# Kernel optimization log

Hardware: AMD Instinct MI355X
Metric: run time of the kernel (lower is better)

Reference implementation:

```python
import jax, jax.numpy as jnp
import numpy as np
from jax import lax

B, L, E_DIM, KSZ = 4, 256, 200, 3
VOCAB, N_LABELS, CORNET = 50000, 28415, 1000
N_EDGES = 454640


def setup_inputs() -> dict:
    key = jax.random.key(0)
    ks = jax.random.split(key, 32)
    w = lambda k, shape, s=0.02: jax.random.normal(k, shape, jnp.float32) * s
    inp = {}
    for i, name in enumerate(['abstract', 'intro', 'method', 'results', 'discuss']):
        inp[name] = jax.random.randint(ks[i], (B, L), 0, VOCAB, dtype=jnp.int32)
    inp['src'] = jax.random.randint(ks[5], (N_EDGES,), 0, N_LABELS, dtype=jnp.int32)
    inp['dst'] = jax.random.randint(ks[6], (N_EDGES,), 0, N_LABELS, dtype=jnp.int32)
    inp['g_node_feature'] = w(ks[7], (N_LABELS, E_DIM))
    inp['emb'] = w(ks[8], (VOCAB, E_DIM))
    for j in range(3):
        inp[f'conv_w{j+1}'] = w(ks[9 + j], (E_DIM, E_DIM, KSZ), 0.05)
        inp[f'conv_b{j+1}'] = jnp.zeros((E_DIM,), jnp.float32)
    inp['gcn_w1'] = w(ks[12], (E_DIM, E_DIM))
    inp['gcn_b1'] = jnp.zeros((E_DIM,), jnp.float32)
    inp['gcn_w2'] = w(ks[13], (E_DIM, E_DIM))
    inp['gcn_b2'] = jnp.zeros((E_DIM,), jnp.float32)
    for blk in (1, 2):
        inp[f'cor_wd{blk}'] = w(ks[13 + blk * 2], (CORNET, N_LABELS), 0.01)
        inp[f'cor_bd{blk}'] = jnp.zeros((CORNET,), jnp.float32)
        inp[f'cor_wc{blk}'] = w(ks[14 + blk * 2], (N_LABELS, CORNET), 0.01)
        inp[f'cor_bc{blk}'] = jnp.zeros((N_LABELS,), jnp.float32)
    return inp


def _conv1d(x, wgt, b, dil):
    # x: [B, C, L]; wgt: [O, I, K]; VALID padding, dilation=dil; SELU (dropout in eval mode)
    y = lax.conv_general_dilated(x, wgt, window_strides=(1,), padding='VALID',
                                 rhs_dilation=(dil,), dimension_numbers=('NCH', 'OIH', 'NCH'))
    return jax.nn.selu(y + b[None, :, None])


def _gcn_agg(feat, src, dst, n):
    # DGL copy_src + sum: h[d] = sum over edges (s->d) of feat[s]
    return jax.ops.segment_sum(feat[src], dst, num_segments=n)


def reference(abstract, intro, method, results, discuss, src, dst, g_node_feature,
              emb, conv_w1, conv_b1, conv_w2, conv_b2, conv_w3, conv_b3,
              gcn_w1, gcn_b1, gcn_w2, gcn_b2,
              cor_wd1, cor_bd1, cor_wc1, cor_bc1, cor_wd2, cor_bd2, cor_wc2, cor_bc2):
    n = g_node_feature.shape[0]
    # LabelNet: two GCN layers (sum-aggregate then linear), relu in between
    h = _gcn_agg(g_node_feature, src, dst, n) @ gcn_w1.T + gcn_b1
    h = jax.nn.relu(h)
    h = _gcn_agg(h, src, dst, n) @ gcn_w2.T + gcn_b2
    label_feature = h + g_node_feature  # [N, E]

    def stream(tokens):
        x = emb[tokens]                      # [B, L, E]
        x = jnp.transpose(x, (0, 2, 1))      # [B, E, L]
        x = _conv1d(x, conv_w1, conv_b1, 1)
        x = _conv1d(x, conv_w2, conv_b2, 2)
        x = _conv1d(x, conv_w3, conv_b3, 3)  # [B, E, L']
        scores = jnp.einsum('bel,ne->bln', x, label_feature)  # [B, L', N]
        atten = jax.nn.softmax(scores, axis=1)                # softmax over L' (dim=1 in torch)
        return jnp.einsum('bel,bln->bne', x, atten)           # [B, N, E]

    context = stream(abstract) + stream(intro) + stream(method) + stream(results) + stream(discuss)
    x_feat = jnp.sum(context * label_feature[None], axis=2)   # [B, N]

    for wd, bd, wc, bc in ((cor_wd1, cor_bd1, cor_wc1, cor_bc1), (cor_wd2, cor_bd2, cor_wc2, cor_bc2)):
        z = jax.nn.sigmoid(x_feat)
        c = jax.nn.elu(z @ wd.T + bd)
        x_feat = c @ wc.T + bc + x_feat
    return x_feat
```

## Files before the change

kernel.cpp:

```cpp
#include <hip/hip_runtime.h>
#include <math.h>

#define E_      200
#define EP      224
#define NL      28415
#define NLP     28416
#define L0      256
#define MROWS   5120
#define CORN    1000
#define NEDGE   454640
#define LOG2E   1.44269504088896f
#define LN2     0.69314718055994531f
#define PREP_TOT 36352
#define SLAB    (MROWS*32)

typedef unsigned short u16;
typedef __attribute__((ext_vector_type(8))) short s16x8;
typedef __attribute__((ext_vector_type(4))) float f32x4;

__device__ __forceinline__ u16 f2b(float f){
    unsigned u = __float_as_uint(f);
    unsigned r = (u + 0x7fffu + ((u >> 16) & 1u)) >> 16;
    return (u16)r;
}
__device__ __forceinline__ float b2f(u16 h){ return __uint_as_float(((unsigned)h) << 16); }

__device__ __forceinline__ float fexp2(float x){
    float r; asm("v_exp_f32 %0, %1" : "=v"(r) : "v"(x)); return r;
}


struct PrepArgs {
    const float* g;   u16* gbf;
    const float* gw1; u16* wdn1;
    const float* gw2; u16* wdn2;
    const float* cw1; u16* wcv1;
    const float* cw2; u16* wcv2;
    const float* cw3; u16* wcv3;
    const int* t0; const int* t1; const int* t2; const int* t3; const int* t4;
    const float* emb; u16* xA;
};

__global__ void k_prep_all(PrepArgs a, const int* __restrict__ dste, int* __restrict__ deg){
    int bid = blockIdx.x;
    int t = threadIdx.x;
    if (bid >= PREP_TOT){
        int e = (bid - PREP_TOT)*256 + t;
        if (e < NEDGE) atomicAdd(&deg[dste[e]], 1);
        return;
    }
    int e = t;
    if (e >= EP) return;
    if (bid < NLP){
        int n = bid;
        float v = (n < NL && e < E_) ? a.g[(size_t)n*E_ + e] : 0.f;
        a.gbf[(size_t)n*EP + e] = f2b(v);
        return;
    }
    bid -= NLP;
    if (bid < 512){
        const float* w = (bid < 256) ? a.gw1 : a.gw2;
        u16* out = (bid < 256) ? a.wdn1 : a.wdn2;
        int o = bid & 255;
        float v = (o < E_ && e < E_) ? w[(size_t)o*E_ + e] : 0.f;
        out[(size_t)o*EP + e] = f2b(v);
        return;
    }
    bid -= 512;
    if (bid < 2304){
        int which = bid / 768;
        const float* w = (which==0) ? a.cw1 : (which==1) ? a.cw2 : a.cw3;
        u16* out = (which==0) ? a.wcv1 : (which==1) ? a.wcv2 : a.wcv3;
        int r = bid - which*768;
        int kk = r >> 8, o = r & 255;
        float v = (o < E_ && e < E_) ? w[((size_t)o*E_ + e)*3 + kk] : 0.f;
        out[(size_t)r*EP + e] = f2b(v);
        return;
    }
    bid -= 2304;
    {
        int chunk = bid >> 8, l = bid & 255, s = chunk >> 2, b = chunk & 3;
        const int* tp = (s==0)?a.t0:(s==1)?a.t1:(s==2)?a.t2:(s==3)?a.t3:a.t4;
        int tok = tp[b*L0 + l];
        float v = (e < E_) ? a.emb[(size_t)tok*E_ + e] : 0.f;
        a.xA[(size_t)bid*EP + e] = f2b(v);
    }
}


__global__ void k_scan1(const int* __restrict__ deg, int* __restrict__ part){
    __shared__ int s[256];
    int t = threadIdx.x;
    int idx = blockIdx.x*256 + t;
    int v = (idx < NLP) ? deg[idx] : 0;
    s[t] = v;
    __syncthreads();
    for (int o = 128; o > 0; o >>= 1){
        if (t < o) s[t] += s[t+o];
        __syncthreads();
    }
    if (t == 0) part[blockIdx.x] = s[0];
}

__global__ void k_scan23(const int* __restrict__ deg, const int* __restrict__ part,
                         int* __restrict__ rowptr, int* __restrict__ cursor){
    __shared__ int s[256];
    __shared__ int sp[128];
    int t = threadIdx.x;
    if (t < 128) sp[t] = (t < 111) ? part[t] : 0;
    __syncthreads();
    for (int o = 1; o < 128; o <<= 1){
        int x = (t < 128 && t >= o) ? sp[t-o] : 0;
        __syncthreads();
        if (t < 128) sp[t] += x;
        __syncthreads();
    }
    int idx = blockIdx.x*256 + t;
    int v = (idx < NLP) ? deg[idx] : 0;
    s[t] = v;
    __syncthreads();
    for (int o = 1; o < 256; o <<= 1){
        int x = (t >= o) ? s[t-o] : 0;
        __syncthreads();
        s[t] += x;
        __syncthreads();
    }
    int bofs = sp[blockIdx.x] - part[blockIdx.x];
    int excl = s[t] - v + bofs;
    if (idx < NLP){ rowptr[idx] = excl; cursor[idx] = excl; }
    if (idx == NLP-1) rowptr[NLP] = excl + v;
}

__global__ void k_scatter(const int* __restrict__ src, const int* __restrict__ dst,
                          int* __restrict__ cursor, int* __restrict__ esrc){
    int e = blockIdx.x*256 + threadIdx.x;
    if (e < NEDGE){
        int p = atomicAdd(&cursor[dst[e]], 1);
        esrc[p] = src[e];
    }
}

__global__ void k_agg(const u16* __restrict__ feat, const int* __restrict__ rp,
                      const int* __restrict__ esrc, u16* __restrict__ out){
    int half = threadIdx.x >> 5;
    int ln   = threadIdx.x & 31;
    int n = blockIdx.x*8 + half;
    if (n >= NL || ln >= 28) return;
    int beg = rp[n], end = rp[n+1];
    float acc0[8] = {0,0,0,0,0,0,0,0};
    float acc1[8] = {0,0,0,0,0,0,0,0};
    int i = beg;
    for (; i + 3 < end; i += 4){
        int s0 = esrc[i], s1 = esrc[i+1], s2 = esrc[i+2], s3 = esrc[i+3];
        s16x8 v0 = *(const s16x8*)(feat + (size_t)s0*EP + ln*8);
        s16x8 v1 = *(const s16x8*)(feat + (size_t)s1*EP + ln*8);
        s16x8 v2 = *(const s16x8*)(feat + (size_t)s2*EP + ln*8);
        s16x8 v3 = *(const s16x8*)(feat + (size_t)s3*EP + ln*8);
#pragma unroll
        for (int j = 0; j < 8; ++j){
            acc0[j] += b2f((u16)v0[j]) + b2f((u16)v2[j]);
            acc1[j] += b2f((u16)v1[j]) + b2f((u16)v3[j]);
        }
    }
    for (; i < end; ++i){
        int s0 = esrc[i];
        s16x8 v0 = *(const s16x8*)(feat + (size_t)s0*EP + ln*8);
#pragma unroll
        for (int j = 0; j < 8; ++j) acc0[j] += b2f((u16)v0[j]);
    }
    s16x8 o;
#pragma unroll
    for (int j = 0; j < 8; ++j) o[j] = (short)f2b(acc0[j] + acc1[j]);
    *(s16x8*)(out + (size_t)n*EP + ln*8) = o;
}


template<int MODE, int BM, int BN, int TRANSP>
__device__ __forceinline__ void gemm_body(char* smem, int bx, int by,
            const u16* __restrict__ A, const u16* __restrict__ B,
            u16* __restrict__ Obf, const float* __restrict__ bias,
            const float* __restrict__ gadd, int dil)
{
    constexpr int NSTEPS = (MODE == 0) ? 21 : 7;
    constexpr int QA = (BM*4)/256, QB = (BN*4)/256, I = BM/64, J = BN/16, WR = BM/4;
    typedef u16 (*AlT)[BM][40];
    typedef u16 (*BlT)[BN][40];
    AlT Al = (AlT)smem;
    BlT Bl = (BlT)(smem + (size_t)2*BM*40*2);

    const int tid  = threadIdx.x;
    const int lane = tid & 63;
    const int w    = tid >> 6;
    const int fr   = lane & 15;
    const int kfo  = (lane >> 4) * 8;
    const int n0     = bx * BN;
    const int m_base = by * BM;

    int ar[QA], ao[QA], brr[QB], bro[QB];
#pragma unroll
    for (int q = 0; q < QA; ++q){ int idx = q*256 + tid; ar[q] = idx >> 2; ao[q] = (idx & 3)*8; }
#pragma unroll
    for (int q = 0; q < QB; ++q){ int idx = q*256 + tid; brr[q] = idx >> 2; bro[q] = (idx & 3)*8; }

    auto aRow = [&](int row, int st)->int {
        if constexpr (MODE == 0){
            int off = (m_base & 255) + row + (st/7)*dil;
            if (off > 255) off = 255;
            return (m_base & ~255) + off;
        } else return m_base + row;
    };
    auto aCol = [&](int st)->int {
        if constexpr (MODE == 0) return (st % 7) * 32; else return st * 32;
    };
    auto bRow = [&](int row, int st)->int {
        if constexpr (MODE == 0) return (st/7)*256 + n0 + row; else return n0 + row;
    };

#pragma unroll
    for (int q = 0; q < QA; ++q){
        s16x8 v = *(const s16x8*)(A + (size_t)aRow(ar[q],0)*EP + aCol(0) + ao[q]);
        *(s16x8*)&Al[0][ar[q]][ao[q]] = v;
    }
#pragma unroll
    for (int q = 0; q < QB; ++q){
        s16x8 v = *(const s16x8*)(B + (size_t)bRow(brr[q],0)*EP + aCol(0) + bro[q]);
        *(s16x8*)&Bl[0][brr[q]][bro[q]] = v;
    }
    __syncthreads();

    f32x4 acc[I][J];
#pragma unroll
    for (int i = 0; i < I; ++i)
#pragma unroll
        for (int j = 0; j < J; ++j){
            f32x4 z = {0.f, 0.f, 0.f, 0.f};
            acc[i][j] = z;
        }

    for (int st = 0; st < NSTEPS; ++st){
        const int cur = st & 1, nxt = cur ^ 1;
        s16x8 ra[QA], rb[QB];
        if (st + 1 < NSTEPS){
#pragma unroll
            for (int q = 0; q < QA; ++q)
                ra[q] = *(const s16x8*)(A + (size_t)aRow(ar[q],st+1)*EP + aCol(st+1) + ao[q]);
#pragma unroll
            for (int q = 0; q < QB; ++q)
                rb[q] = *(const s16x8*)(B + (size_t)bRow(brr[q],st+1)*EP + aCol(st+1) + bro[q]);
        }
        s16x8 af[I], bfr[J];
#pragma unroll
        for (int i = 0; i < I; ++i)
            af[i] = *(const s16x8*)&Al[cur][w*WR + i*16 + fr][kfo];
#pragma unroll
        for (int j = 0; j < J; ++j)
            bfr[j] = *(const s16x8*)&Bl[cur][j*16 + fr][kfo];
#pragma unroll
        for (int i = 0; i < I; ++i)
#pragma unroll
            for (int j = 0; j < J; ++j)
                acc[i][j] = __builtin_amdgcn_mfma_f32_16x16x32_bf16(af[i], bfr[j], acc[i][j], 0, 0, 0);
        if (st + 1 < NSTEPS){
#pragma unroll
            for (int q = 0; q < QA; ++q) *(s16x8*)&Al[nxt][ar[q]][ao[q]] = ra[q];
#pragma unroll
            for (int q = 0; q < QB; ++q) *(s16x8*)&Bl[nxt][brr[q]][bro[q]] = rb[q];
        }
        __syncthreads();
    }

#pragma unroll
    for (int i = 0; i < I; ++i){
#pragma unroll
        for (int j = 0; j < J; ++j){
            int col = n0 + j*16 + fr;
            if (col < EP){
                float bs = (col < E_) ? bias[col] : 0.f;
#pragma unroll
                for (int r = 0; r < 4; ++r){
                    int rowg = m_base + w*WR + i*16 + ((lane >> 4) << 2) + r;
                    float v = acc[i][j][r] + bs;
                    if constexpr (MODE == 1){
                        v = v > 0.f ? v : 0.f;
                    } else if constexpr (MODE == 0){
                        v = v > 0.f ? 1.0507009873554805f * v
                                    : 1.7580993408473766f * (__expf(v) - 1.f);
                    } else {
                        if (col < E_ && rowg < NL) v += gadd[(size_t)rowg*E_ + col];
                        v *= LOG2E;
                    }
                    if constexpr (TRANSP){
                        Obf[(size_t)(col >> 5)*SLAB + (size_t)rowg*32 + (col & 31)] = f2b(v);
                    } else {
                        Obf[(size_t)rowg*EP + col] = f2b(v);
                    }
                }
            }
        }
    }
}

template<int MODE, int BM, int BN, int TRANSP>
__global__ __launch_bounds__(256, 2)
void k_gemm(const u16* __restrict__ A, const u16* __restrict__ B,
            u16* __restrict__ Obf, const float* __restrict__ bias,
            const float* __restrict__ gadd, int dil)
{
    extern __shared__ char smem[];
    gemm_body<MODE,BM,BN,TRANSP>(smem, blockIdx.x, blockIdx.y, A, B, Obf, bias, gadd, dil);
}

template<int MA,int BMa,int BNa, int MB,int BMb,int BNb>
__global__ __launch_bounds__(256, 2)
void k_gemm_dual(int nA, int gxA, int gxB,
            const u16* Aa, const u16* Ba, u16* Oa, const float* ba, const float* ga, int da,
            const u16* Ab, const u16* Bb, u16* Ob, const float* bb, const float* gb, int db)
{
    extern __shared__ char smem[];
    int bid = blockIdx.x;
    if (bid < nA){
        gemm_body<MA,BMa,BNa,0>(smem, bid % gxA, bid / gxA, Aa, Ba, Oa, ba, ga, da);
    } else {
        int b2 = bid - nA;
        gemm_body<MB,BMb,BNb,0>(smem, b2 % gxB, b2 / gxB, Ab, Bb, Ob, bb, gb, db);
    }
}


__global__ __launch_bounds__(256, 2)
void k_scores(const u16* __restrict__ A, const u16* __restrict__ B,
              float* __restrict__ xf, float* __restrict__ zsig)
{
    __shared__ u16 Bl[7][128][40];
    __shared__ float red[2][4][128];

    const int tid  = threadIdx.x;
    const int lane = tid & 63;
    const int w    = tid >> 6;
    const int fr   = lane & 15;
    const int kfo  = (lane >> 4) * 8;
    const int n0   = blockIdx.x * 128;
    const int b    = blockIdx.y;

    const u16* Abase = A + (size_t)(b*256 + w*64 + fr)*32 + kfo;

    s16x8 cur[4], nxt[4];
#pragma unroll
    for (int i = 0; i < 4; ++i)
        cur[i] = *(const s16x8*)(Abase + (size_t)(i*16)*32);

#pragma unroll
    for (int q = 0; q < 14; ++q){
        int v   = q*256 + tid;
        int st  = v >> 9;
        int rem = v & 511;
        int row = rem >> 2;
        int ko  = (rem & 3)*8;
        s16x8 x = *(const s16x8*)(B + (size_t)(n0 + row)*EP + st*32 + ko);
        *(s16x8*)&Bl[st][row][ko] = x;
    }
    __syncthreads();

    float xsum = 0.f;

#pragma unroll
    for (int ci = 0; ci < 5; ++ci){
        const u16* Ac = Abase + (size_t)(ci*4*256)*32;

        f32x4 acc[4][8];
#pragma unroll
        for (int i = 0; i < 4; ++i)
#pragma unroll
            for (int j = 0; j < 8; ++j){
                f32x4 z = {0.f, 0.f, 0.f, 0.f};
                acc[i][j] = z;
            }

#pragma unroll
        for (int st = 0; st < 7; ++st){
            const bool last = (ci == 4) && (st == 6);
            if (!last){
                const u16* An = (st < 6) ? (Ac + (size_t)(st+1)*SLAB)
                                         : (Ac + (size_t)(4*256)*32);
#pragma unroll
                for (int i = 0; i < 4; ++i)
                    nxt[i] = *(const s16x8*)(An + (size_t)(i*16)*32);
            }
            s16x8 bfr[8];
#pragma unroll
            for (int j = 0; j < 8; ++j)
                bfr[j] = *(const s16x8*)&Bl[st][j*16 + fr][kfo];
#pragma unroll
            for (int i = 0; i < 4; ++i)
#pragma unroll
                for (int j = 0; j < 8; ++j)
                    acc[i][j] = __builtin_amdgcn_mfma_f32_16x16x32_bf16(cur[i], bfr[j], acc[i][j], 0, 0, 0);
            if (!last){
#pragma unroll
                for (int i = 0; i < 4; ++i) cur[i] = nxt[i];
            }
        }

        __syncthreads();
#pragma unroll
        for (int j = 0; j < 8; ++j){
            float se = 0.f, sv = 0.f;
#pragma unroll
            for (int i = 0; i < 4; ++i)
#pragma unroll
                for (int r = 0; r < 4; ++r){
                    int row = w*64 + i*16 + ((lane >> 4) << 2) + r;
                    if (row < 244){
                        float v = acc[i][j][r];
                        float e = fexp2(v);
                        se += e; sv += e * v;
                    }
                }
            se += __shfl_xor(se, 16); se += __shfl_xor(se, 32);
            sv += __shfl_xor(sv, 16); sv += __shfl_xor(sv, 32);
            if (lane < 16){
                int cc = j*16 + lane;
                red[0][w][cc] = se;
                red[1][w][cc] = sv;
            }
        }
        __syncthreads();
        if (tid < 128){
            float SE = 0.f, SV = 0.f;
#pragma unroll
            for (int ww = 0; ww < 4; ++ww){
                SE += red[0][ww][tid];
                SV += red[1][ww][tid];
            }
            xsum += SV / SE;
        }
    }

    if (tid < 128){
        int n = n0 + tid;
        if (n < NL){
            float v = xsum * LN2;
            xf[(size_t)b*NLP + n] = v;
            zsig[(size_t)b*NLP + n] = 1.f / (1.f + __expf(-v));
        }
    }
}


__global__ void k_cord(const float* __restrict__ z, const float* __restrict__ wd,
                       const float* __restrict__ bd, float* __restrict__ cbuf){
    int j = blockIdx.x, t = threadIdx.x;
    const float* wr = wd + (size_t)j*NL;
    float a0=0.f, a1=0.f, a2=0.f, a3=0.f;
    for (int n = t; n < NL; n += 256){
        float wv = wr[n];
        a0 += wv * z[n];
        a1 += wv * z[NLP + n];
        a2 += wv * z[2*NLP + n];
        a3 += wv * z[3*NLP + n];
    }
    __shared__ float r[4][256];
    r[0][t]=a0; r[1][t]=a1; r[2][t]=a2; r[3][t]=a3;
    __syncthreads();
    for (int s = 128; s > 0; s >>= 1){
        if (t < s){
            r[0][t]+=r[0][t+s]; r[1][t]+=r[1][t+s];
            r[2][t]+=r[2][t+s]; r[3][t]+=r[3][t+s];
        }
        __syncthreads();
    }
    if (t < 4){
        float v = r[t][0] + bd[j];
        cbuf[(size_t)j*4 + t] = v > 0.f ? v : (__expf(v) - 1.f);
    }
}

template<int FINAL>
__global__ void k_corc(const float* __restrict__ cbuf, const float* __restrict__ wc,
                       const float* __restrict__ bc, float* __restrict__ xf,
                       float* __restrict__ zsig, float* __restrict__ dout){
    __shared__ float4 cl[CORN];
    int t = threadIdx.x;
    for (int i = t; i < CORN; i += 256) cl[i] = ((const float4*)cbuf)[i];
    __syncthreads();
    int w = t >> 6, ln = t & 63;
    for (int r = 0; r < 16; ++r){
        int n = blockIdx.x*64 + w*16 + r;
        if (n >= NL) continue;
        const float4* wr4 = (const float4*)(wc + (size_t)n*CORN);
        float a0=0.f, a1=0.f, a2=0.f, a3=0.f;
#pragma unroll
        for (int it = 0; it < 4; ++it){
            int j4 = ln + it*64;
            if (j4 < 250){
                float4 w4 = wr4[j4];
                float4 c0 = cl[j4*4+0], c1 = cl[j4*4+1], c2 = cl[j4*4+2], c3 = cl[j4*4+3];
                a0 += w4.x*c0.x + w4.y*c1.x + w4.z*c2.x + w4.w*c3.x;
                a1 += w4.x*c0.y + w4.y*c1.y + w4.z*c2.y + w4.w*c3.y;
                a2 += w4.x*c0.z + w4.y*c1.z + w4.z*c2.z + w4.w*c3.z;
                a3 += w4.x*c0.w + w4.y*c1.w + w4.z*c2.w + w4.w*c3.w;
            }
        }
#pragma unroll
        for (int o = 32; o > 0; o >>= 1){
            a0 += __shfl_xor(a0, o);
            a1 += __shfl_xor(a1, o);
            a2 += __shfl_xor(a2, o);
            a3 += __shfl_xor(a3, o);
        }
        if (ln == 0){
            float base = bc[n];
            float v0 = a0 + base + xf[0*(size_t)NLP + n];
            float v1 = a1 + base + xf[1*(size_t)NLP + n];
            float v2 = a2 + base + xf[2*(size_t)NLP + n];
            float v3 = a3 + base + xf[3*(size_t)NLP + n];
            if (FINAL){
                dout[0*(size_t)NL + n] = v0;
                dout[1*(size_t)NL + n] = v1;
                dout[2*(size_t)NL + n] = v2;
                dout[3*(size_t)NL + n] = v3;
            } else {
                xf[0*(size_t)NLP + n] = v0;
                xf[1*(size_t)NLP + n] = v1;
                xf[2*(size_t)NLP + n] = v2;
                xf[3*(size_t)NLP + n] = v3;
                zsig[0*(size_t)NLP + n] = 1.f / (1.f + __expf(-v0));
                zsig[1*(size_t)NLP + n] = 1.f / (1.f + __expf(-v1));
                zsig[2*(size_t)NLP + n] = 1.f / (1.f + __expf(-v2));
                zsig[3*(size_t)NLP + n] = 1.f / (1.f + __expf(-v3));
            }
        }
    }
}


extern "C" void kernel_launch(void* const* d_in, const int* in_sizes, int n_in,
                              void* d_out, int out_size, void* d_ws, size_t ws_size,
                              hipStream_t stream){
    (void)in_sizes; (void)n_in; (void)out_size; (void)ws_size;
    const int* t0 = (const int*)d_in[0];
    const int* t1 = (const int*)d_in[1];
    const int* t2 = (const int*)d_in[2];
    const int* t3 = (const int*)d_in[3];
    const int* t4 = (const int*)d_in[4];
    const int* src = (const int*)d_in[5];
    const int* dst = (const int*)d_in[6];
    const float* g    = (const float*)d_in[7];
    const float* emb  = (const float*)d_in[8];
    const float* cw1 = (const float*)d_in[9];  const float* cb1 = (const float*)d_in[10];
    const float* cw2 = (const float*)d_in[11]; const float* cb2 = (const float*)d_in[12];
    const float* cw3 = (const float*)d_in[13]; const float* cb3 = (const float*)d_in[14];
    const float* gw1 = (const float*)d_in[15]; const float* gb1 = (const float*)d_in[16];
    const float* gw2 = (const float*)d_in[17]; const float* gb2 = (const float*)d_in[18];
    const float* wd1 = (const float*)d_in[19]; const float* bd1 = (const float*)d_in[20];
    const float* wc1 = (const float*)d_in[21]; const float* bc1 = (const float*)d_in[22];
    const float* wd2 = (const float*)d_in[23]; const float* bd2 = (const float*)d_in[24];
    const float* wc2 = (const float*)d_in[25]; const float* bc2 = (const float*)d_in[26];

    char* p = (char*)d_ws;
    auto alloc = [&](size_t bytes)->char* {
        char* r = p;
        p += (bytes + 255) & ~(size_t)255;
        return r;
    };
    u16* gbf = (u16*)alloc((size_t)NLP*EP*2);
    u16* h1  = (u16*)alloc((size_t)NLP*EP*2);
    u16* agg = (u16*)alloc((size_t)NLP*EP*2);
    u16* lfb = (u16*)alloc((size_t)NLP*EP*2);
    u16* xA  = (u16*)alloc((size_t)MROWS*EP*2);
    u16* xB  = (u16*)alloc((size_t)MROWS*EP*2);
    u16* wcv1 = (u16*)alloc((size_t)768*EP*2);
    u16* wcv2 = (u16*)alloc((size_t)768*EP*2);
    u16* wcv3 = (u16*)alloc((size_t)768*EP*2);
    u16* wdn1 = (u16*)alloc((size_t)256*EP*2);
    u16* wdn2 = (u16*)alloc((size_t)256*EP*2);
    float* xf = (float*)alloc((size_t)4*NLP*4);
    float* zb = (float*)alloc((size_t)4*NLP*4);
    float* cb = (float*)alloc((size_t)4*CORN*4);
    int* deg  = (int*)alloc((size_t)NLP*4);
    int* part = (int*)alloc((size_t)128*4);
    int* rp   = (int*)alloc((size_t)(NLP+1)*4);
    int* cur  = (int*)alloc((size_t)NLP*4);
    int* esrc = (int*)alloc((size_t)NEDGE*4);

    hipMemsetAsync(agg + (size_t)NL*EP, 0, (size_t)(NLP-NL)*EP*2, stream);
    hipMemsetAsync(deg, 0, (size_t)NLP*4, stream);

    PrepArgs pa{ g, gbf, gw1, wdn1, gw2, wdn2, cw1, wcv1, cw2, wcv2, cw3, wcv3,
                 t0, t1, t2, t3, t4, emb, xA };
    k_prep_all<<<PREP_TOT + 1776, 256, 0, stream>>>(pa, dst, deg);

    k_scan1<<<111, 256, 0, stream>>>(deg, part);
    k_scan23<<<111, 256, 0, stream>>>(deg, part, rp, cur);
    k_scatter<<<1776, 256, 0, stream>>>(src, dst, cur, esrc);

    const int SM_D = (2*128*40 + 2*64*40)*2;
    const int SM_C = (2*64*40 + 2*64*40)*2;

    k_agg<<<(NL+7)/8, 256, 0, stream>>>(gbf, rp, esrc, agg);
    k_gemm_dual<1,128,64, 0,64,64><<<888+320, 256, SM_D, stream>>>(
        888, 4, 4,
        agg, wdn1, h1, gb1, nullptr, 0,
        xA,  wcv1, xB, cb1, nullptr, 1);
    k_agg<<<(NL+7)/8, 256, 0, stream>>>(h1, rp, esrc, agg);
    k_gemm_dual<2,128,64, 0,64,64><<<888+320, 256, SM_D, stream>>>(
        888, 4, 4,
        agg, wdn2, lfb, gb2, g, 0,
        xB,  wcv2, xA,  cb2, nullptr, 2);
    k_gemm<0,64,64,1><<<dim3(4,80), 256, SM_C, stream>>>(xA, wcv3, xB, cb3, nullptr, 3);

    k_scores<<<dim3(222, 4), 256, 0, stream>>>(xB, lfb, xf, zb);

    k_cord<<<1000, 256, 0, stream>>>(zb, wd1, bd1, cb);
    k_corc<0><<<444, 256, 0, stream>>>(cb, wc1, bc1, xf, zb, nullptr);
    k_cord<<<1000, 256, 0, stream>>>(zb, wd2, bd2, cb);
    k_corc<1><<<444, 256, 0, stream>>>(cb, wc2, bc2, xf, nullptr, (float*)d_out);
}
```

Before: 506.1 us.

## Transpose sigmoid buffer, vectorize and split CorNet down-projection, pre-swizzle scores LDS

The sigmoid activations are now stored interleaved per label as float4, so each label's four batch values load together. k_cord reads weight rows as float4 and splits each row across two blocks, doubling the grid. The two partial sums are combined, with bias and ELU applied, when k_corc loads them. k_scores also stores its B tile in LDS already in MFMA fragment order, giving contiguous per-lane reads and avoiding bank conflicts, at the cost of scattered global loads.

```diff
diff --git a/kernel.cpp b/kernel.cpp
--- a/kernel.cpp
+++ b/kernel.cpp
@@ -13,6 +13,7 @@
 #define LN2     0.69314718055994531f
 #define PREP_TOT 36352
 #define SLAB    (MROWS*32)
+#define NHALF   14208
 
 typedef unsigned short u16;
 typedef __attribute__((ext_vector_type(8))) short s16x8;
@@ -329,9 +330,9 @@
 
 __global__ __launch_bounds__(256, 2)
 void k_scores(const u16* __restrict__ A, const u16* __restrict__ B,
-              float* __restrict__ xf, float* __restrict__ zsig)
+              float* __restrict__ xf, float* __restrict__ zt)
 {
-    __shared__ u16 Bl[7][128][40];
+    __shared__ s16x8 Blf[3584];
     __shared__ float red[2][4][128];
 
     const int tid  = threadIdx.x;
@@ -351,13 +352,13 @@
 
 #pragma unroll
     for (int q = 0; q < 14; ++q){
-        int v   = q*256 + tid;
-        int st  = v >> 9;
-        int rem = v & 511;
-        int row = rem >> 2;
-        int ko  = (rem & 3)*8;
-        s16x8 x = *(const s16x8*)(B + (size_t)(n0 + row)*EP + st*32 + ko);
-        *(s16x8*)&Bl[st][row][ko] = x;
+        int v    = q*256 + tid;
+        int st   = v >> 9;
+        int rem  = v & 511;
+        int j    = rem >> 6;
+        int ln2  = rem & 63;
+        int fr2  = ln2 & 15, kg = ln2 >> 4;
+        Blf[v] = *(const s16x8*)(B + (size_t)(n0 + j*16 + fr2)*EP + st*32 + kg*8);
     }
     __syncthreads();
 
@@ -389,7 +390,7 @@
             s16x8 bfr[8];
 #pragma unroll
             for (int j = 0; j < 8; ++j)
-                bfr[j] = *(const s16x8*)&Bl[st][j*16 + fr][kfo];
+                bfr[j] = Blf[(st*8 + j)*64 + lane];
 #pragma unroll
             for (int i = 0; i < 4; ++i)
 #pragma unroll
@@ -441,24 +442,49 @@
         if (n < NL){
             float v = xsum * LN2;
             xf[(size_t)b*NLP + n] = v;
-            zsig[(size_t)b*NLP + n] = 1.f / (1.f + __expf(-v));
-        }
-    }
-}
-
-
-__global__ void k_cord(const float* __restrict__ z, const float* __restrict__ wd,
-                       const float* __restrict__ bd, float* __restrict__ cbuf){
-    int j = blockIdx.x, t = threadIdx.x;
+            zt[(size_t)n*4 + b] = 1.f / (1.f + __expf(-v));
+        }
+    }
+}
+
+
+__global__ void k_cord(const float4* __restrict__ zt, const float* __restrict__ wd,
+                       float4* __restrict__ pcb){
+    int j = blockIdx.x, h = blockIdx.y, t = threadIdx.x;
     const float* wr = wd + (size_t)j*NL;
+    int base_n = h*NHALF;
+    int end_n  = (h == 0) ? NHALF : NL;
     float a0=0.f, a1=0.f, a2=0.f, a3=0.f;
-    for (int n = t; n < NL; n += 256){
+
+    int mis  = (int)(((size_t)j*NL + base_n) & 3);
+    int lead = (4 - mis) & 3;
+    if (lead > end_n - base_n) lead = end_n - base_n;
+    if (t < lead){
+        int n = base_n + t;
         float wv = wr[n];
-        a0 += wv * z[n];
-        a1 += wv * z[NLP + n];
-        a2 += wv * z[2*NLP + n];
-        a3 += wv * z[3*NLP + n];
-    }
+        float4 zz = zt[n];
+        a0 = wv*zz.x; a1 = wv*zz.y; a2 = wv*zz.z; a3 = wv*zz.w;
+    }
+    int vstart = base_n + lead;
+    int nv = (end_n - vstart) >> 2;
+    const float4* wv4 = (const float4*)(wr + vstart);
+    for (int i = t; i < nv; i += 256){
+        float4 wq = wv4[i];
+        int n = vstart + i*4;
+        float4 z0 = zt[n], z1 = zt[n+1], z2 = zt[n+2], z3 = zt[n+3];
+        a0 += wq.x*z0.x + wq.y*z1.x + wq.z*z2.x + wq.w*z3.x;
+        a1 += wq.x*z0.y + wq.y*z1.y + wq.z*z2.y + wq.w*z3.y;
+        a2 += wq.x*z0.z + wq.y*z1.z + wq.z*z2.z + wq.w*z3.z;
+        a3 += wq.x*z0.w + wq.y*z1.w + wq.z*z2.w + wq.w*z3.w;
+    }
+    int tstart = vstart + nv*4;
+    if (t < end_n - tstart){
+        int n = tstart + t;
+        float wv = wr[n];
+        float4 zz = zt[n];
+        a0 += wv*zz.x; a1 += wv*zz.y; a2 += wv*zz.z; a3 += wv*zz.w;
+    }
+
     __shared__ float r[4][256];
     r[0][t]=a0; r[1][t]=a1; r[2][t]=a2; r[3][t]=a3;
     __syncthreads();
@@ -469,19 +495,29 @@
         }
         __syncthreads();
     }
-    if (t < 4){
-        float v = r[t][0] + bd[j];
-        cbuf[(size_t)j*4 + t] = v > 0.f ? v : (__expf(v) - 1.f);
+    if (t == 0){
+        float4 o; o.x=r[0][0]; o.y=r[1][0]; o.z=r[2][0]; o.w=r[3][0];
+        pcb[(size_t)h*CORN + j] = o;
     }
 }
 
 template<int FINAL>
-__global__ void k_corc(const float* __restrict__ cbuf, const float* __restrict__ wc,
-                       const float* __restrict__ bc, float* __restrict__ xf,
-                       float* __restrict__ zsig, float* __restrict__ dout){
+__global__ void k_corc(const float4* __restrict__ pcb, const float* __restrict__ bd,
+                       const float* __restrict__ wc, const float* __restrict__ bc,
+                       float* __restrict__ xf, float4* __restrict__ zt,
+                       float* __restrict__ dout){
     __shared__ float4 cl[CORN];
     int t = threadIdx.x;
-    for (int i = t; i < CORN; i += 256) cl[i] = ((const float4*)cbuf)[i];
+    for (int i = t; i < CORN; i += 256){
+        float4 s0 = pcb[i], s1 = pcb[CORN + i];
+        float bdv = bd[i];
+        float4 c;
+        c.x = s0.x + s1.x + bdv; c.x = c.x > 0.f ? c.x : (__expf(c.x) - 1.f);
+        c.y = s0.y + s1.y + bdv; c.y = c.y > 0.f ? c.y : (__expf(c.y) - 1.f);
+        c.z = s0.z + s1.z + bdv; c.z = c.z > 0.f ? c.z : (__expf(c.z) - 1.f);
+        c.w = s0.w + s1.w + bdv; c.w = c.w > 0.f ? c.w : (__expf(c.w) - 1.f);
+        cl[i] = c;
+    }
     __syncthreads();
     int w = t >> 6, ln = t & 63;
     for (int r = 0; r < 16; ++r){
@@ -524,10 +560,12 @@
                 xf[1*(size_t)NLP + n] = v1;
                 xf[2*(size_t)NLP + n] = v2;
                 xf[3*(size_t)NLP + n] = v3;
-                zsig[0*(size_t)NLP + n] = 1.f / (1.f + __expf(-v0));
-                zsig[1*(size_t)NLP + n] = 1.f / (1.f + __expf(-v1));
-                zsig[2*(size_t)NLP + n] = 1.f / (1.f + __expf(-v2));
-                zsig[3*(size_t)NLP + n] = 1.f / (1.f + __expf(-v3));
+                float4 zz;
+                zz.x = 1.f / (1.f + __expf(-v0));
+                zz.y = 1.f / (1.f + __expf(-v1));
+                zz.z = 1.f / (1.f + __expf(-v2));
+                zz.w = 1.f / (1.f + __expf(-v3));
+                zt[n] = zz;
             }
         }
     }
@@ -575,8 +613,8 @@
     u16* wdn1 = (u16*)alloc((size_t)256*EP*2);
     u16* wdn2 = (u16*)alloc((size_t)256*EP*2);
     float* xf = (float*)alloc((size_t)4*NLP*4);
-    float* zb = (float*)alloc((size_t)4*NLP*4);
-    float* cb = (float*)alloc((size_t)4*CORN*4);
+    float* zt = (float*)alloc((size_t)NLP*4*4);
+    float* pcb = (float*)alloc((size_t)2*CORN*4*4);
     int* deg  = (int*)alloc((size_t)NLP*4);
     int* part = (int*)alloc((size_t)128*4);
     int* rp   = (int*)alloc((size_t)(NLP+1)*4);
@@ -585,6 +623,7 @@
 
     hipMemsetAsync(agg + (size_t)NL*EP, 0, (size_t)(NLP-NL)*EP*2, stream);
     hipMemsetAsync(deg, 0, (size_t)NLP*4, stream);
+    hipMemsetAsync(zt + (size_t)NL*4, 0, (size_t)(NLP-NL)*4*4, stream);
 
     PrepArgs pa{ g, gbf, gw1, wdn1, gw2, wdn2, cw1, wcv1, cw2, wcv2, cw3, wcv3,
                  t0, t1, t2, t3, t4, emb, xA };
@@ -609,10 +648,10 @@
         xB,  wcv2, xA,  cb2, nullptr, 2);
     k_gemm<0,64,64,1><<<dim3(4,80), 256, SM_C, stream>>>(xA, wcv3, xB, cb3, nullptr, 3);
 
-    k_scores<<<dim3(222, 4), 256, 0, stream>>>(xB, lfb, xf, zb);
-
-    k_cord<<<1000, 256, 0, stream>>>(zb, wd1, bd1, cb);
-    k_corc<0><<<444, 256, 0, stream>>>(cb, wc1, bc1, xf, zb, nullptr);
-    k_cord<<<1000, 256, 0, stream>>>(zb, wd2, bd2, cb);
-    k_corc<1><<<444, 256, 0, stream>>>(cb, wc2, bc2, xf, nullptr, (float*)d_out);
-}
+    k_scores<<<dim3(222, 4), 256, 0, stream>>>(xB, lfb, xf, zt);
+
+    k_cord<<<dim3(CORN, 2), 256, 0, stream>>>((const float4*)zt, wd1, (float4*)pcb);
+    k_corc<0><<<444, 256, 0, stream>>>((const float4*)pcb, bd1, wc1, bc1, xf, (float4*)zt, nullptr);
+    k_cord<<<dim3(CORN, 2), 256, 0, stream>>>((const float4*)zt, wd2, (float4*)pcb);
+    k_corc<1><<<444, 256, 0, stream>>>((const float4*)pcb, bd2, wc2, bc2, xf, nullptr, (float*)d_out);
+}
```

After: 465.6 us, median of 2. 1.09x faster.
